# Performance work log

Measured on AMD Instinct MI355X. Metric: run time of the kernel, lower is better.

The kernel has to match this reference:

```python
import jax, jax.numpy as jnp
import numpy as np
from math import sqrt

EPS = 1e-5


def _head_branch(x, W, b, a, g, be):
    # x: (B,C,T,F); W: (H,O,C); b: (H,O); a: (H,) PReLU; g,be: (H,1,O,1,F)
    y = jnp.einsum('bctf,hoc->hbotf', x, W) + b[:, None, :, None, None]
    y = jnp.where(y > 0, y, a[:, None, None, None, None] * y)  # PReLU
    mean = y.mean(axis=(2, 4), keepdims=True)                  # ChannelNorm over (C,F)
    var = y.var(axis=(2, 4), keepdims=True)
    return (y - mean) / jnp.sqrt(var + EPS) * g + be           # (H,B,O,T,F)


def _proj(x, W, b, a, g, be):
    # x: (B,C,T,F); W: (C,C); b: (C,); a: scalar; g,be: (1,C,1,F)
    y = jnp.einsum('bctf,oc->botf', x, W) + b[None, :, None, None]
    y = jnp.where(y > 0, y, a * y)
    mean = y.mean(axis=(1, 3), keepdims=True)
    var = y.var(axis=(1, 3), keepdims=True)
    return (y - mean) / jnp.sqrt(var + EPS) * g + be


def setup_inputs() -> dict:
    key = jax.random.key(0)
    ks = jax.random.split(key, 8)
    B, C, T, F, H, HID = 4, 64, 1024, 128, 4, 4
    CH = C // H
    x = jax.random.normal(ks[0], (B, C, T, F), dtype=jnp.float32)
    Wq = jax.random.normal(ks[1], (H, HID, C), dtype=jnp.float32) * 0.05
    Wk = jax.random.normal(ks[2], (H, HID, C), dtype=jnp.float32) * 0.05
    Wv = jax.random.normal(ks[3], (H, CH, C), dtype=jnp.float32) * 0.05
    Wp = jax.random.normal(ks[4], (C, C), dtype=jnp.float32) * 0.05
    return {
        'x': x,
        'Wq': Wq, 'bq': jnp.zeros((H, HID)), 'aq': jnp.full((H,), 0.25),
        'gq': jnp.ones((H, 1, HID, 1, F)), 'betaq': jnp.zeros((H, 1, HID, 1, F)),
        'Wk': Wk, 'bk': jnp.zeros((H, HID)), 'ak': jnp.full((H,), 0.25),
        'gk': jnp.ones((H, 1, HID, 1, F)), 'betak': jnp.zeros((H, 1, HID, 1, F)),
        'Wv': Wv, 'bv': jnp.zeros((H, CH)), 'av': jnp.full((H,), 0.25),
        'gv': jnp.ones((H, 1, CH, 1, F)), 'betav': jnp.zeros((H, 1, CH, 1, F)),
        'Wp': Wp, 'bp': jnp.zeros((C,)), 'ap': jnp.float32(0.25),
        'gp': jnp.ones((1, C, 1, F)), 'betap': jnp.zeros((1, C, 1, F)),
    }


def reference(x, Wq, bq, aq, gq, betaq, Wk, bk, ak, gk, betak,
              Wv, bv, av, gv, betav, Wp, bp, ap, gp, betap):
    B, C, T, F = x.shape
    H = Wq.shape[0]
    CH = C // H
    q = _head_branch(x, Wq, bq, aq, gq, betaq)   # (H,B,HID,T,F)
    k = _head_branch(x, Wk, bk, ak, gk, betak)   # (H,B,HID,T,F)
    v = _head_branch(x, Wv, bv, av, gv, betav)   # (H,B,CH,T,F)
    # cat(dim=0) head-major, transpose(1,2), flatten -> (H*B, T, O*F)
    qf = q.transpose(0, 1, 3, 2, 4).reshape(H * B, T, -1)
    kf = k.transpose(0, 1, 3, 2, 4).reshape(H * B, T, -1)
    vf = v.transpose(0, 1, 3, 2, 4).reshape(H * B, T, -1)
    scale = 1.0 / sqrt(qf.shape[-1])
    attn = jax.nn.softmax(jnp.einsum('nqd,nkd->nqk', qf, kf) * scale, axis=-1)
    out = jnp.einsum('nqk,nkd->nqd', attn, vf)   # (H*B, T, CH*F)
    # invert torch's view/transpose chain back to (B,C,T,F)
    out = out.reshape(H, B, T, CH, F).transpose(1, 0, 3, 2, 4).reshape(B, C, T, F)
    out = _proj(out, Wp, bp, ap, gp, betap)
    return out + x
```

## Files before the change

kernel.cpp:

```cpp
#include <hip/hip_runtime.h>
#include <hip/hip_bf16.h>

typedef __attribute__((ext_vector_type(4))) float f32x4;
typedef __attribute__((ext_vector_type(8))) short short8;

__device__ __forceinline__ float bf2f(unsigned short u){
  union { unsigned u32; float f; } v; v.u32 = ((unsigned)u) << 16; return v.f;
}
__device__ __forceinline__ unsigned short f2bf(float f){
  union { float f; unsigned u; } v; v.f = f;
  unsigned x = v.u;
  unsigned r = x + 0x7fffu + ((x >> 16) & 1u);
  return (unsigned short)(r >> 16);
}

__device__ __forceinline__ void gload_lds16(const unsigned short* g, unsigned short* l) {
  __builtin_amdgcn_global_load_lds(
      (const __attribute__((address_space(1))) unsigned int*)g,
      (__attribute__((address_space(3))) unsigned int*)l, 16, 0, 0);
}

__global__ __launch_bounds__(256) void prep_kernel(
    const float* bq, const float* aq, const float* bk, const float* ak,
    const float* bv, const float* av, const float* Wp,
    const float* Wq, const float* Wk, const float* Wv,
    const float* gq, const float* gk, const float* gv,
    const float* beq, const float* bek, const float* bev,
    float* ball, float* aall, float* Wps,
    unsigned short* Wbf, unsigned short* gba, unsigned short* bba)
{
  int idx = blockIdx.x * 256 + threadIdx.x;
  if (idx < 96) {
    int j = idx;
    float b, a;
    if (j < 16)      { b = bq[j];      a = aq[j >> 2]; }
    else if (j < 32) { b = bk[j - 16]; a = ak[(j - 16) >> 2]; }
    else             { b = bv[j - 32]; a = av[(j - 32) >> 4]; }
    ball[j] = b; aall[j] = a;
  } else if (idx < 4192) {
    int r = idx - 96; int o = r >> 6, c = r & 63;
    Wps[c * 64 + o] = Wp[o * 64 + c];
  } else if (idx < 10336) {
    int r = idx - 4192; int j = r >> 6, c = r & 63;
    float w = (j < 16) ? Wq[j * 64 + c] : (j < 32) ? Wk[(j - 16) * 64 + c]
                                                   : Wv[(j - 32) * 64 + c];
    Wbf[j * 64 + c] = f2bf(w);
  } else if (idx < 22624) {
    int r = idx - 10336; int j = r >> 7, f = r & 127;
    float g = (j < 16) ? gq[j * 128 + f] : (j < 32) ? gk[(j - 16) * 128 + f]
                                                    : gv[(j - 32) * 128 + f];
    gba[j * 128 + f] = f2bf(g);
  } else if (idx < 34912) {
    int r = idx - 22624; int j = r >> 7, f = r & 127;
    float be = (j < 16) ? beq[j * 128 + f] : (j < 32) ? bek[(j - 16) * 128 + f]
                                                      : bev[(j - 32) * 128 + f];
    bba[j * 128 + f] = f2bf(be);
  }
}

__global__ __launch_bounds__(256, 3) void qkv_mfma(
    const float* __restrict__ x,
    const unsigned short* __restrict__ Wbf,
    const float* __restrict__ ball, const float* __restrict__ aall,
    const unsigned short* __restrict__ gba, const unsigned short* __restrict__ bba,
    unsigned short* __restrict__ qf, unsigned short* __restrict__ kf,
    unsigned short* __restrict__ vf)
{
  __shared__ unsigned short upool[128 * 64];
  __shared__ float partS[4][96], partQ[4][96];
  __shared__ float gm[12], gi[12];
  __shared__ float bias_l[96], a_l[96];

  int tid = threadIdx.x;
  int t = blockIdx.x, b = blockIdx.y;
  int lane = tid & 63, wave = tid >> 6;
  int l15 = lane & 15, quad = lane >> 4;
  int rowg = wave >> 1, colg = wave & 1;

  if (tid < 96) { bias_l[tid] = ball[tid]; a_l[tid] = aall[tid]; }

  short8 afr[3][2];
  #pragma unroll
  for (int mt3 = 0; mt3 < 3; mt3++) {
    int row = (rowg * 3 + mt3) * 16 + l15;
    #pragma unroll
    for (int ks = 0; ks < 2; ks++)
      afr[mt3][ks] = *(const short8*)(Wbf + row * 64 + ks * 32 + quad * 8);
  }

  unsigned short* xl = upool;
  #pragma unroll
  for (int it = 0; it < 2; it++) {
    int item = it * 256 + tid;
    int cb = item >> 6;
    int np = item & 63;
    int n = np * 2;
    const float* gp = x + ((long)(b * 64 + cb * 8) * 1024 + t) * 128 + n;
    short8 lo, hi;
    #pragma unroll
    for (int w = 0; w < 8; w++) {
      float2 v = *(const float2*)(gp + (long)w * 131072);
      lo[w] = (short)f2bf(v.x);
      hi[w] = (short)f2bf(v.y);
    }
    int perm = cb ^ (np & 7);
    *(short8*)&xl[n * 64 + perm * 8]       = lo;
    *(short8*)&xl[(n + 1) * 64 + perm * 8] = hi;
  }
  __syncthreads();

  f32x4 acc[3][4];
  #pragma unroll
  for (int mt3 = 0; mt3 < 3; mt3++)
    #pragma unroll
    for (int nt = 0; nt < 4; nt++)
      acc[mt3][nt] = {0.f, 0.f, 0.f, 0.f};

  int nb = colg * 64;
  #pragma unroll
  for (int ks = 0; ks < 2; ks++)
    #pragma unroll
    for (int nt = 0; nt < 4; nt++) {
      int n = nb + nt * 16 + l15;
      int perm = (ks * 4 + quad) ^ ((n >> 1) & 7);
      short8 bfrag = *(const short8*)&xl[n * 64 + perm * 8];
      #pragma unroll
      for (int mt3 = 0; mt3 < 3; mt3++)
        acc[mt3][nt] = __builtin_amdgcn_mfma_f32_16x16x32_bf16(
            afr[mt3][ks], bfrag, acc[mt3][nt], 0, 0, 0);
    }

  #pragma unroll
  for (int mt3 = 0; mt3 < 3; mt3++)
    #pragma unroll
    for (int r = 0; r < 4; r++) {
      int j = (rowg * 3 + mt3) * 16 + quad * 4 + r;
      float bb = bias_l[j], aa = a_l[j];
      #pragma unroll
      for (int nt = 0; nt < 4; nt++) {
        float v = acc[mt3][nt][r] + bb;
        acc[mt3][nt][r] = v > 0.f ? v : aa * v;
      }
      float s  = acc[mt3][0][r] + acc[mt3][1][r] + acc[mt3][2][r] + acc[mt3][3][r];
      float q2 = acc[mt3][0][r]*acc[mt3][0][r] + acc[mt3][1][r]*acc[mt3][1][r]
               + acc[mt3][2][r]*acc[mt3][2][r] + acc[mt3][3][r]*acc[mt3][3][r];
      #pragma unroll
      for (int m = 1; m <= 8; m <<= 1) {
        s  += __shfl_xor(s,  m, 64);
        q2 += __shfl_xor(q2, m, 64);
      }
      if (l15 == 0) { partS[wave][j] = s; partQ[wave][j] = q2; }
    }
  __syncthreads();

  if (tid < 12) {
    int g = tid;
    int r0 = (g < 4) ? g * 4 : (g < 8) ? 16 + (g - 4) * 4 : 32 + (g - 8) * 16;
    int nr = (g < 8) ? 4 : 16;
    int rw = (r0 < 48) ? 0 : 2;
    float S = 0.f, Q = 0.f;
    for (int w2 = 0; w2 < 2; w2++)
      for (int r = 0; r < nr; r++) { S += partS[rw + w2][r0 + r]; Q += partQ[rw + w2][r0 + r]; }
    float cnt = (float)(nr * 128);
    float mean = S / cnt;
    float var = fmaxf(Q / cnt - mean * mean, 0.f);
    gm[g] = mean;
    gi[g] = rsqrtf(var + 1e-5f);
  }

  unsigned short* yl = upool;
  int ch = tid & 15, jrow = tid >> 4;

  #pragma unroll
  for (int half = 0; half < 2; half++) {
    if (rowg == half) {
      #pragma unroll
      for (int mt3 = 0; mt3 < 3; mt3++)
        #pragma unroll
        for (int nt = 0; nt < 4; nt++) {
          int n = nb + nt * 16 + l15;
          #pragma unroll
          for (int r = 0; r < 4; r++) {
            int jrel = mt3 * 16 + quad * 4 + r;
            yl[jrel * 136 + n] = f2bf(acc[mt3][nt][r]);
          }
        }
    }
    __syncthreads();

    #pragma unroll
    for (int itj = 0; itj < 3; itj++) {
      int jrel = itj * 16 + jrow;
      int j = half * 48 + jrel;
      int f = ch * 8;
      short8 y8 = *(const short8*)&yl[jrel * 136 + f];
      int g = (j < 16) ? (j >> 2) : (j < 32) ? 4 + ((j - 16) >> 2) : 8 + ((j - 32) >> 4);
      float mean = gm[g], inv = gi[g];
      unsigned short* dst;
      if (j < 16) {
        int h = j >> 2, o = j & 3;
        dst = qf + (((long)(h * 4 + b) * 1024 + t) * 512 + o * 128 + f);
      } else if (j < 32) {
        int jo = j - 16; int h = jo >> 2, o = jo & 3;
        dst = kf + (((long)(h * 4 + b) * 1024 + t) * 512 + o * 128 + f);
      } else {
        int jo = j - 32; int h = jo >> 4, o = jo & 15;
        dst = vf + (((long)(h * 4 + b) * 1024 + t) * 2048 + o * 128 + f);
      }
      short8 g8 = *(const short8*)(gba + j * 128 + f);
      short8 b8 = *(const short8*)(bba + j * 128 + f);
      short8 o8;
      #pragma unroll
      for (int i = 0; i < 8; i++)
        o8[i] = (short)f2bf((bf2f((unsigned short)y8[i]) - mean) * inv
                            * bf2f((unsigned short)g8[i]) + bf2f((unsigned short)b8[i]));
      *(short8*)dst = o8;
    }
    if (half == 0) __syncthreads();
  }
}

__global__ __launch_bounds__(256) void transpose_v(
    const unsigned short* __restrict__ vf, unsigned short* __restrict__ vfT)
{
  __shared__ unsigned short tile[64][65];
  int n = blockIdx.z;
  int d0 = blockIdx.x * 64, t0 = blockIdx.y * 64;
  int tid = threadIdx.x;
  int cr = tid >> 4, cc = (tid & 15) * 4;

  const unsigned short* src = vf + ((long)n * 1024 + t0) * 2048 + d0;
  #pragma unroll
  for (int i = 0; i < 4; i++) {
    int r = cr + i * 16;
    ushort4 u = *(const ushort4*)(src + (long)r * 2048 + cc);
    tile[r][cc + 0] = u.x; tile[r][cc + 1] = u.y;
    tile[r][cc + 2] = u.z; tile[r][cc + 3] = u.w;
  }
  __syncthreads();
  unsigned short* dst = vfT + ((long)n * 2048 + d0) * 1024 + t0;
  #pragma unroll
  for (int i = 0; i < 4; i++) {
    int r = cr + i * 16;
    ushort4 u;
    u.x = tile[cc + 0][r]; u.y = tile[cc + 1][r];
    u.z = tile[cc + 2][r]; u.w = tile[cc + 3][r];
    *(ushort4*)(dst + (long)r * 1024 + cc) = u;
  }
}

__global__ __launch_bounds__(256) void gemm_bt(
    const unsigned short* __restrict__ A, const unsigned short* __restrict__ B,
    unsigned short* __restrict__ CbA, unsigned short* __restrict__ CbB,
    int M, int N, int K, long sA, long sB, long sC, float scale)
{
  __shared__ unsigned short smem[128 * 136];
  unsigned short* As = smem;
  unsigned short* Bs = smem + 128 * 64;
  int tid = threadIdx.x;

  int gx = gridDim.x, gy = gridDim.y;
  int bid = blockIdx.x + gx * (blockIdx.y + gy * blockIdx.z);
  int nwg = gx * gy * (int)gridDim.z;
  int cpx = nwg >> 3;
  int tile = (bid & 7) * cpx + (bid >> 3);
  int tx = tile % gx, trem = tile / gx;
  int ty = trem % gy, z = trem / gy;

  int m0 = ty * 128, n0 = tx * 128;
  const unsigned short* Ab = A + (long)z * sA + (long)m0 * K;
  const unsigned short* Bb = B + (long)z * sB + (long)n0 * K;
  int lane = tid & 63, wave = tid >> 6;
  int wm = (wave >> 1) * 64, wn = (wave & 1) * 64;
  int l15 = lane & 15, quad = lane >> 4;

  f32x4 acc[4][4];
  #pragma unroll
  for (int i = 0; i < 4; i++)
    #pragma unroll
    for (int j = 0; j < 4; j++) acc[i][j] = {0.f, 0.f, 0.f, 0.f};

  int srow8 = lane >> 3;
  int sck   = (lane & 7) ^ srow8;

  for (int k0 = 0; k0 < K; k0 += 64) {
    #pragma unroll
    for (int it = 0; it < 4; it++) {
      int R = it * 32 + wave * 8;
      int row = R + srow8;
      gload_lds16(Ab + (long)row * K + k0 + sck * 8, &As[R * 64]);
      gload_lds16(Bb + (long)row * K + k0 + sck * 8, &Bs[R * 64]);
    }
    __syncthreads();
    #pragma unroll
    for (int ks = 0; ks < 2; ks++) {
      short8 af[4], bfr[4];
      #pragma unroll
      for (int i = 0; i < 4; i++) {
        int row = wm + i * 16 + l15;
        af[i] = *(const short8*)&As[row * 64 + ((ks * 4 + quad) ^ (row & 7)) * 8];
      }
      #pragma unroll
      for (int j = 0; j < 4; j++) {
        int row = wn + j * 16 + l15;
        bfr[j] = *(const short8*)&Bs[row * 64 + ((ks * 4 + quad) ^ (row & 7)) * 8];
      }
      #pragma unroll
      for (int i = 0; i < 4; i++)
        #pragma unroll
        for (int j = 0; j < 4; j++)
          acc[i][j] = __builtin_amdgcn_mfma_f32_16x16x32_bf16(af[i], bfr[j], acc[i][j], 0, 0, 0);
    }
    __syncthreads();
  }

  #pragma unroll
  for (int i = 0; i < 4; i++)
    #pragma unroll
    for (int j = 0; j < 4; j++) {
      int row0 = wm + i * 16 + quad * 4;
      int col = wn + j * 16 + l15;
      #pragma unroll
      for (int r = 0; r < 4; r++)
        smem[(row0 + r) * 136 + col] = f2bf(acc[i][j][r] * scale);
    }
  __syncthreads();
  unsigned short* Cz = (z < 8) ? (CbA + (long)z * sC) : (CbB + (long)(z - 8) * sC);
  #pragma unroll
  for (int it = 0; it < 8; it++) {
    int chunk = it * 256 + tid;
    int row = chunk >> 4, c8 = (chunk & 15) * 8;
    *(short8*)(Cz + (long)(m0 + row) * N + n0 + c8) = *(const short8*)&smem[row * 136 + c8];
  }
}

__global__ __launch_bounds__(256) void softmax_kernel(unsigned short* __restrict__ P)
{
  __shared__ float red[4];
  __shared__ float bmax, bsum;
  int row = blockIdx.x, z = blockIdx.y, tid = threadIdx.x;
  unsigned short* p = P + ((long)z * 1024 + row) * 1024;
  ushort4 u = *(ushort4*)(p + tid * 4);
  float v0 = bf2f(u.x), v1 = bf2f(u.y), v2 = bf2f(u.z), v3 = bf2f(u.w);

  float m = fmaxf(fmaxf(v0, v1), fmaxf(v2, v3));
  #pragma unroll
  for (int s = 1; s <= 32; s <<= 1) m = fmaxf(m, __shfl_xor(m, s, 64));
  if ((tid & 63) == 0) red[tid >> 6] = m;
  __syncthreads();
  if (tid == 0) bmax = fmaxf(fmaxf(red[0], red[1]), fmaxf(red[2], red[3]));
  __syncthreads();
  m = bmax;

  float e0 = __expf(v0 - m), e1 = __expf(v1 - m), e2 = __expf(v2 - m), e3 = __expf(v3 - m);
  float s = e0 + e1 + e2 + e3;
  #pragma unroll
  for (int k = 1; k <= 32; k <<= 1) s += __shfl_xor(s, k, 64);
  if ((tid & 63) == 0) red[tid >> 6] = s;
  __syncthreads();
  if (tid == 0) bsum = red[0] + red[1] + red[2] + red[3];
  __syncthreads();
  float inv = 1.0f / bsum;

  u.x = f2bf(e0 * inv); u.y = f2bf(e1 * inv);
  u.z = f2bf(e2 * inv); u.w = f2bf(e3 * inv);
  *(ushort4*)(p + tid * 4) = u;
}

__global__ __launch_bounds__(256) void proj_kernel(
    float* __restrict__ io,
    const unsigned short* __restrict__ ofA, const unsigned short* __restrict__ ofB,
    const float* __restrict__ Wps,
    const float* __restrict__ bp, const float* __restrict__ ap,
    const float* __restrict__ gp, const float* __restrict__ bep,
    const float* __restrict__ x)
{
  __shared__ float xl[64 * 128];
  __shared__ float wl[64 * 64];
  __shared__ float redS[4], redQ[4];
  __shared__ float smean, sinv;

  int tid = threadIdx.x;
  int t = blockIdx.x, b = blockIdx.y;

  #pragma unroll
  for (int i = 0; i < 4; i++) {
    int chunk = i * 256 + tid;
    int h = chunk >> 8;
    int dvc = (chunk & 255) * 8;
    int z = h * 4 + b;
    const unsigned short* base =
        (z < 8) ? (ofA + (long)z * 2097152) : (ofB + (long)(z - 8) * 2097152);
    short8 v = *(const short8*)(base + (long)t * 2048 + dvc);
    int c = h * 16 + (dvc >> 7);
    int f = dvc & 127;
    #pragma unroll
    for (int e = 0; e < 8; e++) xl[c * 128 + f + e] = bf2f((unsigned short)v[e]);
  }
  #pragma unroll
  for (int i = 0; i < 4; i++) {
    int id = tid + i * 256;
    ((f32x4*)wl)[id] = ((const f32x4*)Wps)[id];
  }
  __syncthreads();

  int fblk = tid & 31, rblk = tid >> 5;
  int f0 = fblk * 4, r0 = rblk * 8;

  float acc[8][4];
  #pragma unroll
  for (int rr = 0; rr < 8; rr++)
    #pragma unroll
    for (int ff = 0; ff < 4; ff++) acc[rr][ff] = 0.f;

  for (int c = 0; c < 64; c++) {
    f32x4 xv = *(const f32x4*)&xl[c * 128 + f0];
    f32x4 w0 = *(const f32x4*)&wl[c * 64 + r0];
    f32x4 w1 = *(const f32x4*)&wl[c * 64 + r0 + 4];
    #pragma unroll
    for (int rr = 0; rr < 4; rr++) {
      #pragma unroll
      for (int ff = 0; ff < 4; ff++) {
        acc[rr][ff]     += w0[rr] * xv[ff];
        acc[rr + 4][ff] += w1[rr] * xv[ff];
      }
    }
  }

  float aval = ap[0];
  #pragma unroll
  for (int rr = 0; rr < 8; rr++) {
    float bb = bp[r0 + rr];
    #pragma unroll
    for (int ff = 0; ff < 4; ff++) {
      float v = acc[rr][ff] + bb;
      acc[rr][ff] = v > 0.f ? v : aval * v;
    }
  }

  float s = 0.f, sq = 0.f;
  #pragma unroll
  for (int rr = 0; rr < 8; rr++)
    #pragma unroll
    for (int ff = 0; ff < 4; ff++) { s += acc[rr][ff]; sq += acc[rr][ff] * acc[rr][ff]; }
  #pragma unroll
  for (int m = 1; m <= 32; m <<= 1) { s += __shfl_xor(s, m, 64); sq += __shfl_xor(sq, m, 64); }
  if ((tid & 63) == 0) { redS[tid >> 6] = s; redQ[tid >> 6] = sq; }
  __syncthreads();
  if (tid == 0) {
    float S = redS[0] + redS[1] + redS[2] + redS[3];
    float Q = redQ[0] + redQ[1] + redQ[2] + redQ[3];
    float mean = S / 8192.0f;
    float var = fmaxf(Q / 8192.0f - mean * mean, 0.f);
    smean = mean; sinv = rsqrtf(var + 1e-5f);
  }
  __syncthreads();
  float mean = smean, inv = sinv;

  const float* xb = x + ((long)(b * 64) * 1024 + t) * 128;
  #pragma unroll
  for (int rr = 0; rr < 8; rr++) {
    int c = r0 + rr;
    f32x4 g4 = *(const f32x4*)(gp + c * 128 + f0);
    f32x4 b4 = *(const f32x4*)(bep + c * 128 + f0);
    f32x4 x4 = *(const f32x4*)(xb + (long)c * 131072 + f0);
    f32x4 o;
    o[0] = (acc[rr][0] - mean) * inv * g4[0] + b4[0] + x4[0];
    o[1] = (acc[rr][1] - mean) * inv * g4[1] + b4[1] + x4[1];
    o[2] = (acc[rr][2] - mean) * inv * g4[2] + b4[2] + x4[2];
    o[3] = (acc[rr][3] - mean) * inv * g4[3] + b4[3] + x4[3];
    *(f32x4*)(io + ((long)(b * 64 + c) * 1024 + t) * 128 + f0) = o;
  }
}

extern "C" void kernel_launch(void* const* d_in, const int* in_sizes, int n_in,
                              void* d_out, int out_size, void* d_ws, size_t ws_size,
                              hipStream_t stream)
{
  const float* x   = (const float*)d_in[0];
  const float* Wq  = (const float*)d_in[1];
  const float* bq  = (const float*)d_in[2];
  const float* aq  = (const float*)d_in[3];
  const float* gq  = (const float*)d_in[4];
  const float* beq = (const float*)d_in[5];
  const float* Wk  = (const float*)d_in[6];
  const float* bk  = (const float*)d_in[7];
  const float* ak  = (const float*)d_in[8];
  const float* gk  = (const float*)d_in[9];
  const float* bek = (const float*)d_in[10];
  const float* Wv  = (const float*)d_in[11];
  const float* bv  = (const float*)d_in[12];
  const float* av  = (const float*)d_in[13];
  const float* gv  = (const float*)d_in[14];
  const float* bev = (const float*)d_in[15];
  const float* Wp  = (const float*)d_in[16];
  const float* bp  = (const float*)d_in[17];
  const float* ap  = (const float*)d_in[18];
  const float* gp  = (const float*)d_in[19];
  const float* bep = (const float*)d_in[20];
  float* out = (float*)d_out;

  char* ws = (char*)d_ws;
  size_t off = 0;
  auto alloc = [&](size_t n) { size_t o = off; off += (n + 255) & ~(size_t)255; return o; };

  float* ball = (float*)(ws + alloc(96 * 4));
  float* aall = (float*)(ws + alloc(96 * 4));
  float* Wps  = (float*)(ws + alloc(4096 * 4));
  unsigned short* Wbf = (unsigned short*)(ws + alloc(6144 * 2));
  unsigned short* gba = (unsigned short*)(ws + alloc(12288 * 2));
  unsigned short* bba = (unsigned short*)(ws + alloc(12288 * 2));
  unsigned short* qf  = (unsigned short*)(ws + alloc((size_t)16 * 1024 * 512 * 2));
  unsigned short* kf  = (unsigned short*)(ws + alloc((size_t)16 * 1024 * 512 * 2));
  unsigned short* vf  = (unsigned short*)(ws + alloc((size_t)16 * 1024 * 2048 * 2));
  unsigned short* vfT = (unsigned short*)(ws + alloc((size_t)16 * 1024 * 2048 * 2));
  unsigned short* P   = vf;
  unsigned short* ofA = qf;
  unsigned short* ofB = (unsigned short*)((char*)vf + (size_t)32 * 1024 * 1024);

  prep_kernel<<<137, 256, 0, stream>>>(bq, aq, bk, ak, bv, av, Wp,
                                       Wq, Wk, Wv, gq, gk, gv, beq, bek, bev,
                                       ball, aall, Wps, Wbf, gba, bba);

  qkv_mfma<<<dim3(1024, 4), 256, 0, stream>>>(
      x, Wbf, ball, aall, gba, bba, qf, kf, vf);

  transpose_v<<<dim3(32, 16, 16), 256, 0, stream>>>(vf, vfT);

  gemm_bt<<<dim3(8, 8, 16), 256, 0, stream>>>(
      qf, kf, P, P + (long)8 * 1024 * 1024, 1024, 1024, 512,
      (long)1024 * 512, (long)1024 * 512, (long)1024 * 1024,
      0.04419417382f );

  softmax_kernel<<<dim3(1024, 16), 256, 0, stream>>>(P);

  gemm_bt<<<dim3(16, 8, 16), 256, 0, stream>>>(
      P, vfT, ofA, ofB, 1024, 2048, 1024,
      (long)1024 * 1024, (long)2048 * 1024, (long)1024 * 2048, 1.0f);

  proj_kernel<<<dim3(1024, 4), 256, 0, stream>>>(out, ofA, ofB, Wps, bp, ap, gp, bep, x);
}
```

Measured before the change: 517.9 us.

## Restructure qkv kernel: batched loads, packed bf16 converts, swapped MFMA operands, single-pass LDS

In the QKV projection kernel, all sixteen x loads are issued before any conversion, and the software bf16 rounding is replaced with the hardware v_cvt_pk_bf16_f32 instruction plus byte permutes. The MFMA operands are swapped so each lane holds one output channel across its accumulator registers. This lets the PReLU and statistics reduction use fewer shuffles and lets each lane write packed 8-byte LDS stores. The LDS staging buffer is doubled so both row halves are written at once, removing one barrier. The trade-off is more LDS per block, which may lower occupancy.

```diff
diff --git a/kernel.cpp b/kernel.cpp
--- a/kernel.cpp
+++ b/kernel.cpp
@@ -12,6 +12,11 @@
   unsigned x = v.u;
   unsigned r = x + 0x7fffu + ((x >> 16) & 1u);
   return (unsigned short)(r >> 16);
+}
+__device__ __forceinline__ unsigned cvtpk(float a, float b){
+  unsigned r;
+  asm("v_cvt_pk_bf16_f32 %0, %1, %2" : "=v"(r) : "v"(a), "v"(b));
+  return r;
 }
 
 __device__ __forceinline__ void gload_lds16(const unsigned short* g, unsigned short* l) {
@@ -66,7 +71,7 @@
     unsigned short* __restrict__ qf, unsigned short* __restrict__ kf,
     unsigned short* __restrict__ vf)
 {
-  __shared__ unsigned short upool[128 * 64];
+  __shared__ unsigned short upool[2 * 48 * 136];
   __shared__ float partS[4][96], partQ[4][96];
   __shared__ float gm[12], gi[12];
   __shared__ float bias_l[96], a_l[96];
@@ -79,42 +84,57 @@
 
   if (tid < 96) { bias_l[tid] = ball[tid]; a_l[tid] = aall[tid]; }
 
-  short8 afr[3][2];
-  #pragma unroll
-  for (int mt3 = 0; mt3 < 3; mt3++) {
-    int row = (rowg * 3 + mt3) * 16 + l15;
+  short8 wfr[3][2];
+  #pragma unroll
+  for (int mt = 0; mt < 3; mt++) {
+    int row = (rowg * 3 + mt) * 16 + l15;
     #pragma unroll
     for (int ks = 0; ks < 2; ks++)
-      afr[mt3][ks] = *(const short8*)(Wbf + row * 64 + ks * 32 + quad * 8);
+      wfr[mt][ks] = *(const short8*)(Wbf + row * 64 + ks * 32 + quad * 8);
   }
 
   unsigned short* xl = upool;
-  #pragma unroll
-  for (int it = 0; it < 2; it++) {
-    int item = it * 256 + tid;
-    int cb = item >> 6;
-    int np = item & 63;
-    int n = np * 2;
-    const float* gp = x + ((long)(b * 64 + cb * 8) * 1024 + t) * 128 + n;
-    short8 lo, hi;
-    #pragma unroll
-    for (int w = 0; w < 8; w++) {
-      float2 v = *(const float2*)(gp + (long)w * 131072);
-      lo[w] = (short)f2bf(v.x);
-      hi[w] = (short)f2bf(v.y);
-    }
-    int perm = cb ^ (np & 7);
-    *(short8*)&xl[n * 64 + perm * 8]       = lo;
-    *(short8*)&xl[(n + 1) * 64 + perm * 8] = hi;
+  {
+    float2 v[16];
+    #pragma unroll
+    for (int it = 0; it < 2; it++) {
+      int item = it * 256 + tid;
+      int cb = item >> 6;
+      int np = item & 63;
+      const float* gp = x + ((long)(b * 64 + cb * 8) * 1024 + t) * 128 + np * 2;
+      #pragma unroll
+      for (int w = 0; w < 8; w++)
+        v[it * 8 + w] = *(const float2*)(gp + (long)w * 131072);
+    }
+    #pragma unroll
+    for (int it = 0; it < 2; it++) {
+      int item = it * 256 + tid;
+      int cb = item >> 6;
+      int np = item & 63;
+      int n = np * 2;
+      unsigned pk[8];
+      #pragma unroll
+      for (int w = 0; w < 8; w++)
+        pk[w] = cvtpk(v[it * 8 + w].x, v[it * 8 + w].y);
+      union { unsigned u[4]; short8 s; } lo, hi;
+      #pragma unroll
+      for (int k = 0; k < 4; k++) {
+        lo.u[k] = __builtin_amdgcn_perm(pk[2 * k + 1], pk[2 * k], 0x05040100u);
+        hi.u[k] = __builtin_amdgcn_perm(pk[2 * k + 1], pk[2 * k], 0x07060302u);
+      }
+      int perm_s = cb ^ (np & 7);
+      *(short8*)&xl[n * 64 + perm_s * 8]       = lo.s;
+      *(short8*)&xl[(n + 1) * 64 + perm_s * 8] = hi.s;
+    }
   }
   __syncthreads();
 
   f32x4 acc[3][4];
   #pragma unroll
-  for (int mt3 = 0; mt3 < 3; mt3++)
+  for (int mt = 0; mt < 3; mt++)
     #pragma unroll
     for (int nt = 0; nt < 4; nt++)
-      acc[mt3][nt] = {0.f, 0.f, 0.f, 0.f};
+      acc[mt][nt] = {0.f, 0.f, 0.f, 0.f};
 
   int nb = colg * 64;
   #pragma unroll
@@ -122,35 +142,32 @@
     #pragma unroll
     for (int nt = 0; nt < 4; nt++) {
       int n = nb + nt * 16 + l15;
-      int perm = (ks * 4 + quad) ^ ((n >> 1) & 7);
-      short8 bfrag = *(const short8*)&xl[n * 64 + perm * 8];
-      #pragma unroll
-      for (int mt3 = 0; mt3 < 3; mt3++)
-        acc[mt3][nt] = __builtin_amdgcn_mfma_f32_16x16x32_bf16(
-            afr[mt3][ks], bfrag, acc[mt3][nt], 0, 0, 0);
-    }
-
-  #pragma unroll
-  for (int mt3 = 0; mt3 < 3; mt3++)
-    #pragma unroll
-    for (int r = 0; r < 4; r++) {
-      int j = (rowg * 3 + mt3) * 16 + quad * 4 + r;
-      float bb = bias_l[j], aa = a_l[j];
-      #pragma unroll
-      for (int nt = 0; nt < 4; nt++) {
-        float v = acc[mt3][nt][r] + bb;
-        acc[mt3][nt][r] = v > 0.f ? v : aa * v;
+      int perm_s = (ks * 4 + quad) ^ ((n >> 1) & 7);
+      short8 xfrag = *(const short8*)&xl[n * 64 + perm_s * 8];
+      #pragma unroll
+      for (int mt = 0; mt < 3; mt++)
+        acc[mt][nt] = __builtin_amdgcn_mfma_f32_16x16x32_bf16(
+            xfrag, wfr[mt][ks], acc[mt][nt], 0, 0, 0);
+    }
+
+  #pragma unroll
+  for (int mt = 0; mt < 3; mt++) {
+    int j = (rowg * 3 + mt) * 16 + l15;
+    float bb = bias_l[j], aa = a_l[j];
+    float s = 0.f, q2 = 0.f;
+    #pragma unroll
+    for (int nt = 0; nt < 4; nt++)
+      #pragma unroll
+      for (int r = 0; r < 4; r++) {
+        float v = acc[mt][nt][r] + bb;
+        v = v > 0.f ? v : aa * v;
+        acc[mt][nt][r] = v;
+        s += v; q2 += v * v;
       }
-      float s  = acc[mt3][0][r] + acc[mt3][1][r] + acc[mt3][2][r] + acc[mt3][3][r];
-      float q2 = acc[mt3][0][r]*acc[mt3][0][r] + acc[mt3][1][r]*acc[mt3][1][r]
-               + acc[mt3][2][r]*acc[mt3][2][r] + acc[mt3][3][r]*acc[mt3][3][r];
-      #pragma unroll
-      for (int m = 1; m <= 8; m <<= 1) {
-        s  += __shfl_xor(s,  m, 64);
-        q2 += __shfl_xor(q2, m, 64);
-      }
-      if (l15 == 0) { partS[wave][j] = s; partQ[wave][j] = q2; }
-    }
+    s  += __shfl_xor(s, 16, 64);  s += __shfl_xor(s, 32, 64);
+    q2 += __shfl_xor(q2, 16, 64); q2 += __shfl_xor(q2, 32, 64);
+    if (quad == 0) { partS[wave][j] = s; partQ[wave][j] = q2; }
+  }
   __syncthreads();
 
   if (tid < 12) {
@@ -168,32 +185,31 @@
     gi[g] = rsqrtf(var + 1e-5f);
   }
 
-  unsigned short* yl = upool;
+  unsigned short* ylw = upool + rowg * (48 * 136);
+  #pragma unroll
+  for (int mt = 0; mt < 3; mt++) {
+    int jrel = mt * 16 + l15;
+    #pragma unroll
+    for (int nt = 0; nt < 4; nt++) {
+      int f = nb + nt * 16 + quad * 4;
+      union { unsigned u[2]; uint2 u2; } p;
+      p.u[0] = cvtpk(acc[mt][nt][0], acc[mt][nt][1]);
+      p.u[1] = cvtpk(acc[mt][nt][2], acc[mt][nt][3]);
+      *(uint2*)&ylw[jrel * 136 + f] = p.u2;
+    }
+  }
+  __syncthreads();
+
   int ch = tid & 15, jrow = tid >> 4;
-
   #pragma unroll
   for (int half = 0; half < 2; half++) {
-    if (rowg == half) {
-      #pragma unroll
-      for (int mt3 = 0; mt3 < 3; mt3++)
-        #pragma unroll
-        for (int nt = 0; nt < 4; nt++) {
-          int n = nb + nt * 16 + l15;
-          #pragma unroll
-          for (int r = 0; r < 4; r++) {
-            int jrel = mt3 * 16 + quad * 4 + r;
-            yl[jrel * 136 + n] = f2bf(acc[mt3][nt][r]);
-          }
-        }
-    }
-    __syncthreads();
-
+    const unsigned short* ylr = upool + half * (48 * 136);
     #pragma unroll
     for (int itj = 0; itj < 3; itj++) {
       int jrel = itj * 16 + jrow;
       int j = half * 48 + jrel;
       int f = ch * 8;
-      short8 y8 = *(const short8*)&yl[jrel * 136 + f];
+      short8 y8 = *(const short8*)&ylr[jrel * 136 + f];
       int g = (j < 16) ? (j >> 2) : (j < 32) ? 4 + ((j - 16) >> 2) : 8 + ((j - 32) >> 4);
       float mean = gm[g], inv = gi[g];
       unsigned short* dst;
@@ -209,14 +225,17 @@
       }
       short8 g8 = *(const short8*)(gba + j * 128 + f);
       short8 b8 = *(const short8*)(bba + j * 128 + f);
-      short8 o8;
+      float o_[8];
       #pragma unroll
       for (int i = 0; i < 8; i++)
-        o8[i] = (short)f2bf((bf2f((unsigned short)y8[i]) - mean) * inv
-                            * bf2f((unsigned short)g8[i]) + bf2f((unsigned short)b8[i]));
-      *(short8*)dst = o8;
-    }
-    if (half == 0) __syncthreads();
+        o_[i] = (bf2f((unsigned short)y8[i]) - mean) * inv
+                * bf2f((unsigned short)g8[i]) + bf2f((unsigned short)b8[i]);
+      union { unsigned u[4]; short8 s; } ou;
+      #pragma unroll
+      for (int i = 0; i < 4; i++)
+        ou.u[i] = cvtpk(o_[2 * i], o_[2 * i + 1]);
+      *(short8*)dst = ou.s;
+    }
   }
 }
 
```

After: 504.6 us. -2.6%, faster.
